# Performance work log

Hardware: AMD Instinct MI355X
Metric: run time of the kernel (lower is better)

## Reference

```python
import jax, jax.numpy as jnp
import numpy as np

EPS = 1e-5

def _layernorm(x, gamma, beta):
    mu = jnp.mean(x, axis=-1, keepdims=True)
    var = jnp.mean(jnp.square(x - mu), axis=-1, keepdims=True)
    return (x - mu) * jax.lax.rsqrt(var + EPS) * gamma + beta

def setup_inputs() -> dict:
    key = jax.random.key(0)
    kx, kw = jax.random.split(key)
    N, D, BIT = 65536, 1024, 64
    X = jax.random.normal(kx, (N, D), dtype=jnp.float32)
    # xavier_uniform with gain=0.5 for weight [BIT, D]
    limit = 0.5 * np.sqrt(6.0 / (D + BIT))
    W = jax.random.uniform(kw, (BIT, D), minval=-limit, maxval=limit, dtype=jnp.float32)
    b = jnp.zeros((BIT,), dtype=jnp.float32)
    ln1_g = jnp.ones((D,), dtype=jnp.float32)
    ln1_b = jnp.zeros((D,), dtype=jnp.float32)
    ln2_g = jnp.ones((BIT,), dtype=jnp.float32)
    ln2_b = jnp.zeros((BIT,), dtype=jnp.float32)
    return {"X": X, "W": W, "b": b, "ln1_g": ln1_g, "ln1_b": ln1_b, "ln2_g": ln2_g, "ln2_b": ln2_b}

def reference(X, W, b, ln1_g, ln1_b, ln2_g, ln2_b):
    # LayerNorm -> Linear -> LayerNorm
    xn = _layernorm(X, ln1_g, ln1_b)                       # [N, D]
    logits = jnp.einsum('nd,bd->nb', xn, W) + b            # [N, BIT]
    logits = _layernorm(logits, ln2_g, ln2_b)
    # mean-center over batch, tanh, sign-binarize
    logits = logits - jnp.mean(logits, axis=0, keepdims=True)
    H = jnp.tanh(0.5 * logits)
    B = jnp.where(H >= 0.0, jnp.int8(1), jnp.int8(-1))
    return H, B
```

## Files before the change

kernel.cpp:

```cpp
#include <hip/hip_runtime.h>
#include <stdint.h>

#define N_ROWS 65536
#define D_IN   1024
#define NBIT   64
#define LN_EPS 1e-5f

typedef __attribute__((ext_vector_type(8))) _Float16 f16x8;
typedef __attribute__((ext_vector_type(4))) float f32x4;

__device__ __forceinline__ void gload_lds16(const void* g, void* l) {
    __builtin_amdgcn_global_load_lds(
        (const __attribute__((address_space(1))) uint32_t*)g,
        (__attribute__((address_space(3))) uint32_t*)l, 16, 0, 0);
}

__device__ __forceinline__ f32x4 mfma16(f16x8 a, f16x8 b, f32x4 c) {
    return __builtin_amdgcn_mfma_f32_16x16x32_f16(a, b, c, 0, 0, 0);
}

__device__ __forceinline__ void do_tstep(float4 x0, float4 x1,
        const _Float16* bhp, f32x4* acc_h, f32x4* acc_m, f32x4* acc_ll,
        float& sum, float& sumsq) {
    float xs[8] = {x0.x, x0.y, x0.z, x0.w, x1.x, x1.y, x1.z, x1.w};
    f16x8 ahi, alo;
#pragma unroll
    for (int j = 0; j < 8; ++j) {
        float xv = xs[j];
        sum += xv;
        sumsq = fmaf(xv, xv, sumsq);
        _Float16 h = (_Float16)xv;
        ahi[j] = h;
        alo[j] = (_Float16)((xv - (float)h) * 2048.0f);
    }
#pragma unroll
    for (int nt = 0; nt < 4; ++nt) {
        f16x8 bh = *(const f16x8*)(bhp + nt * 512);
        f16x8 bl = *(const f16x8*)(bhp + 4096 + nt * 512);
        acc_h[nt]  = mfma16(ahi, bh, acc_h[nt]);
        acc_m[nt]  = mfma16(ahi, bl, acc_m[nt]);
        acc_m[nt]  = mfma16(alo, bh, acc_m[nt]);
        acc_ll[nt] = mfma16(alo, bl, acc_ll[nt]);
    }
}

__global__ void prep_kernel(const float* __restrict__ W, const float* __restrict__ bias,
                            const float* __restrict__ g1, const float* __restrict__ b1,
                            _Float16* __restrict__ whi, _Float16* __restrict__ wlo,
                            float* __restrict__ u, float* __restrict__ v) {
    int bit = blockIdx.x;
    int t   = threadIdx.x;
    int nt  = bit >> 4, bl = bit & 15;
    float su = 0.f, sv = 0.f;
    for (int d = t; d < D_IN; d += 256) {
        float w  = W[bit * D_IN + d];
        float gw = w * g1[d];
        su += gw;
        sv += w * b1[d];
        int kt = d >> 5, gg = (d >> 3) & 3, j = d & 7;
        size_t idx = (((size_t)(kt * 4 + nt)) * 64 + gg * 16 + bl) * 8 + j;
        _Float16 h = (_Float16)gw;
        whi[idx] = h;
        wlo[idx] = (_Float16)((gw - (float)h) * 2048.0f);
    }
    __shared__ float s1[256], s2[256];
    s1[t] = su; s2[t] = sv;
    __syncthreads();
    for (int off = 128; off > 0; off >>= 1) {
        if (t < off) { s1[t] += s1[t + off]; s2[t] += s2[t + off]; }
        __syncthreads();
    }
    if (t == 0) { u[bit] = s1[0]; v[bit] = s2[0] + bias[bit]; }
}

__global__ void __launch_bounds__(256) main_kernel(
        const float* __restrict__ X,
        const _Float16* __restrict__ whi, const _Float16* __restrict__ wlo,
        const float* __restrict__ u, const float* __restrict__ v,
        const float* __restrict__ g2, const float* __restrict__ b2,
        float* __restrict__ L, float* __restrict__ P) {
    __shared__ _Float16 lw[2][8192];
    int tid  = threadIdx.x;
    int wid  = tid >> 6, lane = tid & 63;
    int g    = lane >> 4, r16 = lane & 15;
    int row_base = blockIdx.x * 64 + wid * 16;

    const float* xrow = X + (size_t)(row_base + r16) * D_IN + g * 8;

    const _Float16* gbase = ((wid & 2) ? wlo : whi) + (wid & 1) * 2048 + lane * 8;
    const int lofs = ((wid & 2) ? 4096 : 0) + (wid & 1) * 2048;

#define STAGEW(cc, buf) do {                                         \
        const _Float16* gs_ = gbase + (cc) * 4096;                   \
        _Float16* ld_ = &lw[buf][lofs];                              \
        gload_lds16(gs_,         ld_);                               \
        gload_lds16(gs_ + 512,   ld_ + 512);                         \
        gload_lds16(gs_ + 1024,  ld_ + 1024);                        \
        gload_lds16(gs_ + 1536,  ld_ + 1536);                        \
    } while (0)

#define PREFX(cc, r0, r1, r2, r3) do {                               \
        const float* xp_ = xrow + (cc) * 64;                         \
        r0 = *(const float4*)(xp_);                                  \
        r1 = *(const float4*)(xp_ + 4);                              \
        r2 = *(const float4*)(xp_ + 32);                             \
        r3 = *(const float4*)(xp_ + 36);                             \
    } while (0)

    f32x4 acc_h0[4], acc_h1[4], acc_m[4], acc_ll[4];
#pragma unroll
    for (int nt = 0; nt < 4; ++nt) {
        acc_h0[nt] = (f32x4){0.f, 0.f, 0.f, 0.f};
        acc_h1[nt] = (f32x4){0.f, 0.f, 0.f, 0.f};
        acc_m[nt]  = (f32x4){0.f, 0.f, 0.f, 0.f};
        acc_ll[nt] = (f32x4){0.f, 0.f, 0.f, 0.f};
    }
    float sum = 0.f, sumsq = 0.f;
    float4 xa0, xa1, xa2, xa3, xb0, xb1, xb2, xb3;

    PREFX(0, xa0, xa1, xa2, xa3);
    STAGEW(0, 0);
    __syncthreads();

    for (int c2 = 0; c2 < 8; ++c2) {
        int c = 2 * c2;
        PREFX(c + 1, xb0, xb1, xb2, xb3);
        STAGEW(c + 1, 1);
        {
            const _Float16* bhp = &lw[0][0] + lane * 8;
            do_tstep(xa0, xa1, bhp,        acc_h0, acc_m, acc_ll, sum, sumsq);
            do_tstep(xa2, xa3, bhp + 2048, acc_h1, acc_m, acc_ll, sum, sumsq);
        }
        __syncthreads();
        if (c2 < 7) {
            PREFX(c + 2, xa0, xa1, xa2, xa3);
            STAGEW(c + 2, 0);
        }
        {
            const _Float16* bhp = &lw[1][0] + lane * 8;
            do_tstep(xb0, xb1, bhp,        acc_h0, acc_m, acc_ll, sum, sumsq);
            do_tstep(xb2, xb3, bhp + 2048, acc_h1, acc_m, acc_ll, sum, sumsq);
        }
        __syncthreads();
    }

    sum   += __shfl_xor(sum, 16);   sum   += __shfl_xor(sum, 32);
    sumsq += __shfl_xor(sumsq, 16); sumsq += __shfl_xor(sumsq, 32);
    float mu   = sum * (1.f / 1024.f);
    float var  = sumsq * (1.f / 1024.f) - mu * mu;
    float rstd = rsqrtf(var + LN_EPS);

    float uv[4], vv[4], g2v[4], b2v[4];
#pragma unroll
    for (int nt = 0; nt < 4; ++nt) {
        int bitc = nt * 16 + r16;
        uv[nt] = u[bitc]; vv[nt] = v[bitc]; g2v[nt] = g2[bitc]; b2v[nt] = b2[bitc];
    }
    float mu_m[4], rs_m[4];
#pragma unroll
    for (int reg = 0; reg < 4; ++reg) {
        int m = g * 4 + reg;
        mu_m[reg] = __shfl(mu, m);
        rs_m[reg] = __shfl(rstd, m);
    }

    float lg[4][4];
#pragma unroll
    for (int nt = 0; nt < 4; ++nt)
#pragma unroll
        for (int reg = 0; reg < 4; ++reg) {
            float dot = (acc_h0[nt][reg] + acc_h1[nt][reg])
                      + acc_m[nt][reg] * (1.0f / 2048.0f)
                      + acc_ll[nt][reg] * (1.0f / 4194304.0f);
            lg[nt][reg] = rs_m[reg] * dot - rs_m[reg] * mu_m[reg] * uv[nt] + vv[nt];
        }

#pragma unroll
    for (int reg = 0; reg < 4; ++reg) {
        float s1 = lg[0][reg] + lg[1][reg] + lg[2][reg] + lg[3][reg];
        float s2 = lg[0][reg]*lg[0][reg] + lg[1][reg]*lg[1][reg]
                 + lg[2][reg]*lg[2][reg] + lg[3][reg]*lg[3][reg];
#pragma unroll
        for (int m = 1; m <= 8; m <<= 1) {
            s1 += __shfl_xor(s1, m);
            s2 += __shfl_xor(s2, m);
        }
        float mean = s1 * (1.f / 64.f);
        float va   = s2 * (1.f / 64.f) - mean * mean;
        float rs2  = rsqrtf(va + LN_EPS);
#pragma unroll
        for (int nt = 0; nt < 4; ++nt)
            lg[nt][reg] = (lg[nt][reg] - mean) * rs2 * g2v[nt] + b2v[nt];
    }

#pragma unroll
    for (int reg = 0; reg < 4; ++reg) {
        size_t row = (size_t)(row_base + g * 4 + reg);
#pragma unroll
        for (int nt = 0; nt < 4; ++nt)
            L[row * 64 + nt * 16 + r16] = lg[nt][reg];
    }

#pragma unroll
    for (int nt = 0; nt < 4; ++nt) {
        float cs = lg[nt][0] + lg[nt][1] + lg[nt][2] + lg[nt][3];
        cs += __shfl_xor(cs, 16);
        cs += __shfl_xor(cs, 32);
        if (g == 0)
            P[(size_t)(nt * 16 + r16) * 4096 + blockIdx.x * 4 + wid] = cs;
    }
#undef STAGEW
#undef PREFX
}

__global__ void reduce_kernel(const float* __restrict__ P, float* __restrict__ cm) {
    int bit = blockIdx.x, t = threadIdx.x;
    float s = 0.f;
    for (int p = t; p < 4096; p += 256) s += P[(size_t)bit * 4096 + p];
    __shared__ float sh[256];
    sh[t] = s;
    __syncthreads();
    for (int off = 128; off > 0; off >>= 1) {
        if (t < off) sh[t] += sh[t + off];
        __syncthreads();
    }
    if (t == 0) cm[bit] = sh[0] * (1.f / (float)N_ROWS);
}

__global__ void final_kernel(const float* __restrict__ L, const float* __restrict__ cm,
                             float* __restrict__ out) {
    __shared__ float cms[64];
    if (threadIdx.x < 64) cms[threadIdx.x] = cm[threadIdx.x];
    __syncthreads();
    const float4* L4 = (const float4*)L;
    float4* H4 = (float4*)out;
    float4* B4 = (float4*)(out + (size_t)N_ROWS * NBIT);
    int total = N_ROWS * NBIT / 4;
    for (int i = blockIdx.x * blockDim.x + threadIdx.x; i < total;
         i += gridDim.x * blockDim.x) {
        float4 x = L4[i];
        int bb = (i & 15) * 4;
        float4 h, bo;
        h.x = tanhf(0.5f * (x.x - cms[bb + 0]));
        h.y = tanhf(0.5f * (x.y - cms[bb + 1]));
        h.z = tanhf(0.5f * (x.z - cms[bb + 2]));
        h.w = tanhf(0.5f * (x.w - cms[bb + 3]));
        bo.x = h.x >= 0.f ? 1.f : -1.f;
        bo.y = h.y >= 0.f ? 1.f : -1.f;
        bo.z = h.z >= 0.f ? 1.f : -1.f;
        bo.w = h.w >= 0.f ? 1.f : -1.f;
        H4[i] = h;
        B4[i] = bo;
    }
}

extern "C" void kernel_launch(void* const* d_in, const int* in_sizes, int n_in,
                              void* d_out, int out_size, void* d_ws, size_t ws_size,
                              hipStream_t stream) {
    (void)in_sizes; (void)n_in; (void)out_size; (void)ws_size;
    const float* X  = (const float*)d_in[0];
    const float* W  = (const float*)d_in[1];
    const float* bb = (const float*)d_in[2];
    const float* g1 = (const float*)d_in[3];
    const float* b1 = (const float*)d_in[4];
    const float* g2 = (const float*)d_in[5];
    const float* b2 = (const float*)d_in[6];

    char* ws = (char*)d_ws;
    _Float16* whi = (_Float16*)ws;
    _Float16* wlo = (_Float16*)(ws + 131072);
    float* u  = (float*)(ws + 262144);
    float* v  = (float*)(ws + 266240);
    float* P  = (float*)(ws + 270336);
    float* cm = (float*)(ws + 270336 + 64 * 4096 * 4);

    float* out = (float*)d_out;
    float* L   = out + (size_t)N_ROWS * NBIT;

    prep_kernel<<<64, 256, 0, stream>>>(W, bb, g1, b1, whi, wlo, u, v);
    main_kernel<<<1024, 256, 0, stream>>>(X, whi, wlo, u, v, g2, b2, L, P);
    reduce_kernel<<<64, 256, 0, stream>>>(P, cm);
    final_kernel<<<2048, 256, 0, stream>>>(L, cm, out);
}
```

Before: 98.09 us.

## Restructure main loop pipeline with explicit vmcnt waits and sched barriers

Rewrites the double-buffered K loop so X register prefetch runs two chunks ahead and W LDS staging one chunk ahead. Full __syncthreads (which drain all outstanding loads) are replaced with s_waitcnt vmcnt(4) plus s_barrier, so the next chunk's X loads can stay in flight across the barrier. Sched barriers pin the instruction order so the compiler cannot undo the overlap. This relies on precise vmcnt accounting of the outstanding loads; a wrong count would race on LDS.

```diff
diff --git a/kernel.cpp b/kernel.cpp
--- a/kernel.cpp
+++ b/kernel.cpp
@@ -107,6 +107,8 @@
         r3 = *(const float4*)(xp_ + 36);                             \
     } while (0)
 
+#define SB0 __builtin_amdgcn_sched_barrier(0)
+
     f32x4 acc_h0[4], acc_h1[4], acc_m[4], acc_ll[4];
 #pragma unroll
     for (int nt = 0; nt < 4; ++nt) {
@@ -119,29 +121,47 @@
     float4 xa0, xa1, xa2, xa3, xb0, xb1, xb2, xb3;
 
     PREFX(0, xa0, xa1, xa2, xa3);
+    PREFX(1, xb0, xb1, xb2, xb3);
     STAGEW(0, 0);
-    __syncthreads();
-
-    for (int c2 = 0; c2 < 8; ++c2) {
+    SB0;
+    asm volatile("s_waitcnt vmcnt(0)" ::: "memory");
+    __builtin_amdgcn_s_barrier();
+
+#define ITER(c, xr0, xr1, xr2, xr3) do {                                      \
+        STAGEW((c) + 1, ((c) + 1) & 1);                                       \
+        SB0;                                                                  \
+        {                                                                     \
+            const _Float16* bhp = &lw[(c) & 1][0] + lane * 8;                 \
+            do_tstep(xr0, xr1, bhp,        acc_h0, acc_m, acc_ll, sum, sumsq);\
+            do_tstep(xr2, xr3, bhp + 2048, acc_h1, acc_m, acc_ll, sum, sumsq);\
+        }                                                                     \
+        SB0;                                                                  \
+        PREFX((c) + 2, xr0, xr1, xr2, xr3);                                   \
+        SB0;                                                                  \
+        asm volatile("s_waitcnt vmcnt(4)" ::: "memory");                      \
+        __builtin_amdgcn_s_barrier();                                         \
+    } while (0)
+
+    for (int c2 = 0; c2 < 7; ++c2) {
         int c = 2 * c2;
-        PREFX(c + 1, xb0, xb1, xb2, xb3);
-        STAGEW(c + 1, 1);
-        {
-            const _Float16* bhp = &lw[0][0] + lane * 8;
-            do_tstep(xa0, xa1, bhp,        acc_h0, acc_m, acc_ll, sum, sumsq);
-            do_tstep(xa2, xa3, bhp + 2048, acc_h1, acc_m, acc_ll, sum, sumsq);
-        }
-        __syncthreads();
-        if (c2 < 7) {
-            PREFX(c + 2, xa0, xa1, xa2, xa3);
-            STAGEW(c + 2, 0);
-        }
-        {
-            const _Float16* bhp = &lw[1][0] + lane * 8;
-            do_tstep(xb0, xb1, bhp,        acc_h0, acc_m, acc_ll, sum, sumsq);
-            do_tstep(xb2, xb3, bhp + 2048, acc_h1, acc_m, acc_ll, sum, sumsq);
-        }
-        __syncthreads();
+        ITER(c,     xa0, xa1, xa2, xa3);
+        ITER(c + 1, xb0, xb1, xb2, xb3);
+    }
+
+    STAGEW(15, 1);
+    SB0;
+    {
+        const _Float16* bhp = &lw[0][0] + lane * 8;
+        do_tstep(xa0, xa1, bhp,        acc_h0, acc_m, acc_ll, sum, sumsq);
+        do_tstep(xa2, xa3, bhp + 2048, acc_h1, acc_m, acc_ll, sum, sumsq);
+    }
+    SB0;
+    asm volatile("s_waitcnt vmcnt(0)" ::: "memory");
+    __builtin_amdgcn_s_barrier();
+    {
+        const _Float16* bhp = &lw[1][0] + lane * 8;
+        do_tstep(xb0, xb1, bhp,        acc_h0, acc_m, acc_ll, sum, sumsq);
+        do_tstep(xb2, xb3, bhp + 2048, acc_h1, acc_m, acc_ll, sum, sumsq);
     }
 
     sum   += __shfl_xor(sum, 16);   sum   += __shfl_xor(sum, 32);
@@ -211,6 +231,8 @@
     }
 #undef STAGEW
 #undef PREFX
+#undef ITER
+#undef SB0
 }
 
 __global__ void reduce_kernel(const float* __restrict__ P, float* __restrict__ cm) {
```

Measured after the change: 98.21 us. About the same (+0.1%).

## Use 1024-thread blocks sharing staged weights, drop X register prefetch, add nontemporal loads/stores

Applied to the files above, without the earlier changes.

The main kernel now runs 256 blocks of 1024 threads (16 waves, 256 rows each), so each staged weight chunk in LDS is reused by four times as many rows and each thread issues only one LDS-bound load per chunk. The explicit X register double-buffering is replaced by direct nontemporal loads inside the loop, and L/H/B writes and L reads use nontemporal hints. This cuts weight staging traffic and register pressure, but X load latency is no longer hidden by software prefetch and relies on 16 waves per block instead. The larger blocks may also reduce occupancy flexibility and make each per-chunk barrier more costly.

```diff
diff --git a/kernel.cpp b/kernel.cpp
--- a/kernel.cpp
+++ b/kernel.cpp
@@ -15,14 +15,18 @@
         (__attribute__((address_space(3))) uint32_t*)l, 16, 0, 0);
 }
 
+__device__ __forceinline__ f32x4 ntload4(const float* p) {
+    return __builtin_nontemporal_load((const f32x4*)p);
+}
+
 __device__ __forceinline__ f32x4 mfma16(f16x8 a, f16x8 b, f32x4 c) {
     return __builtin_amdgcn_mfma_f32_16x16x32_f16(a, b, c, 0, 0, 0);
 }
 
-__device__ __forceinline__ void do_tstep(float4 x0, float4 x1,
+__device__ __forceinline__ void do_tstep(f32x4 x0, f32x4 x1,
         const _Float16* bhp, f32x4* acc_h, f32x4* acc_m, f32x4* acc_ll,
         float& sum, float& sumsq) {
-    float xs[8] = {x0.x, x0.y, x0.z, x0.w, x1.x, x1.y, x1.z, x1.w};
+    float xs[8] = {x0[0], x0[1], x0[2], x0[3], x1[0], x1[1], x1[2], x1[3]};
     f16x8 ahi, alo;
 #pragma unroll
     for (int j = 0; j < 8; ++j) {
@@ -73,7 +77,7 @@
     if (t == 0) { u[bit] = s1[0]; v[bit] = s2[0] + bias[bit]; }
 }
 
-__global__ void __launch_bounds__(256) main_kernel(
+__global__ void __launch_bounds__(1024) main_kernel(
         const float* __restrict__ X,
         const _Float16* __restrict__ whi, const _Float16* __restrict__ wlo,
         const float* __restrict__ u, const float* __restrict__ v,
@@ -83,29 +87,14 @@
     int tid  = threadIdx.x;
     int wid  = tid >> 6, lane = tid & 63;
     int g    = lane >> 4, r16 = lane & 15;
-    int row_base = blockIdx.x * 64 + wid * 16;
+    int row_base = blockIdx.x * 256 + wid * 16;
 
     const float* xrow = X + (size_t)(row_base + r16) * D_IN + g * 8;
 
-    const _Float16* gbase = ((wid & 2) ? wlo : whi) + (wid & 1) * 2048 + lane * 8;
-    const int lofs = ((wid & 2) ? 4096 : 0) + (wid & 1) * 2048;
-
-#define STAGEW(cc, buf) do {                                         \
-        const _Float16* gs_ = gbase + (cc) * 4096;                   \
-        _Float16* ld_ = &lw[buf][lofs];                              \
-        gload_lds16(gs_,         ld_);                               \
-        gload_lds16(gs_ + 512,   ld_ + 512);                         \
-        gload_lds16(gs_ + 1024,  ld_ + 1024);                        \
-        gload_lds16(gs_ + 1536,  ld_ + 1536);                        \
-    } while (0)
-
-#define PREFX(cc, r0, r1, r2, r3) do {                               \
-        const float* xp_ = xrow + (cc) * 64;                         \
-        r0 = *(const float4*)(xp_);                                  \
-        r1 = *(const float4*)(xp_ + 4);                              \
-        r2 = *(const float4*)(xp_ + 32);                             \
-        r3 = *(const float4*)(xp_ + 36);                             \
-    } while (0)
+    const _Float16* gsrc = ((wid & 8) ? wlo : whi) + (wid & 7) * 512 + (size_t)lane * 8;
+    const int ldst = ((wid & 8) ? 4096 : 0) + (wid & 7) * 512;
+
+#define STAGEW(cc, buf) gload_lds16(gsrc + (size_t)(cc) * 4096, &lw[buf][ldst])
 
     f32x4 acc_h0[4], acc_h1[4], acc_m[4], acc_ll[4];
 #pragma unroll
@@ -116,31 +105,20 @@
         acc_ll[nt] = (f32x4){0.f, 0.f, 0.f, 0.f};
     }
     float sum = 0.f, sumsq = 0.f;
-    float4 xa0, xa1, xa2, xa3, xb0, xb1, xb2, xb3;
-
-    PREFX(0, xa0, xa1, xa2, xa3);
+
     STAGEW(0, 0);
     __syncthreads();
 
-    for (int c2 = 0; c2 < 8; ++c2) {
-        int c = 2 * c2;
-        PREFX(c + 1, xb0, xb1, xb2, xb3);
-        STAGEW(c + 1, 1);
-        {
-            const _Float16* bhp = &lw[0][0] + lane * 8;
-            do_tstep(xa0, xa1, bhp,        acc_h0, acc_m, acc_ll, sum, sumsq);
-            do_tstep(xa2, xa3, bhp + 2048, acc_h1, acc_m, acc_ll, sum, sumsq);
-        }
-        __syncthreads();
-        if (c2 < 7) {
-            PREFX(c + 2, xa0, xa1, xa2, xa3);
-            STAGEW(c + 2, 0);
-        }
-        {
-            const _Float16* bhp = &lw[1][0] + lane * 8;
-            do_tstep(xb0, xb1, bhp,        acc_h0, acc_m, acc_ll, sum, sumsq);
-            do_tstep(xb2, xb3, bhp + 2048, acc_h1, acc_m, acc_ll, sum, sumsq);
-        }
+    for (int c = 0; c < 16; ++c) {
+        if (c < 15) STAGEW(c + 1, (c + 1) & 1);
+        int t = c * 2;
+        f32x4 x00 = ntload4(xrow + t * 32);
+        f32x4 x01 = ntload4(xrow + t * 32 + 4);
+        f32x4 x10 = ntload4(xrow + t * 32 + 32);
+        f32x4 x11 = ntload4(xrow + t * 32 + 36);
+        const _Float16* bhp = &lw[c & 1][0] + lane * 8;
+        do_tstep(x00, x01, bhp,        acc_h0, acc_m, acc_ll, sum, sumsq);
+        do_tstep(x10, x11, bhp + 2048, acc_h1, acc_m, acc_ll, sum, sumsq);
         __syncthreads();
     }
 
@@ -198,7 +176,7 @@
         size_t row = (size_t)(row_base + g * 4 + reg);
 #pragma unroll
         for (int nt = 0; nt < 4; ++nt)
-            L[row * 64 + nt * 16 + r16] = lg[nt][reg];
+            __builtin_nontemporal_store(lg[nt][reg], &L[row * 64 + nt * 16 + r16]);
     }
 
 #pragma unroll
@@ -207,10 +185,9 @@
         cs += __shfl_xor(cs, 16);
         cs += __shfl_xor(cs, 32);
         if (g == 0)
-            P[(size_t)(nt * 16 + r16) * 4096 + blockIdx.x * 4 + wid] = cs;
+            P[(size_t)(nt * 16 + r16) * 4096 + blockIdx.x * 16 + wid] = cs;
     }
 #undef STAGEW
-#undef PREFX
 }
 
 __global__ void reduce_kernel(const float* __restrict__ P, float* __restrict__ cm) {
@@ -232,25 +209,22 @@
     __shared__ float cms[64];
     if (threadIdx.x < 64) cms[threadIdx.x] = cm[threadIdx.x];
     __syncthreads();
-    const float4* L4 = (const float4*)L;
-    float4* H4 = (float4*)out;
-    float4* B4 = (float4*)(out + (size_t)N_ROWS * NBIT);
+    const f32x4* L4 = (const f32x4*)L;
+    f32x4* H4 = (f32x4*)out;
+    f32x4* B4 = (f32x4*)(out + (size_t)N_ROWS * NBIT);
     int total = N_ROWS * NBIT / 4;
     for (int i = blockIdx.x * blockDim.x + threadIdx.x; i < total;
          i += gridDim.x * blockDim.x) {
-        float4 x = L4[i];
+        f32x4 x = __builtin_nontemporal_load(&L4[i]);
         int bb = (i & 15) * 4;
-        float4 h, bo;
-        h.x = tanhf(0.5f * (x.x - cms[bb + 0]));
-        h.y = tanhf(0.5f * (x.y - cms[bb + 1]));
-        h.z = tanhf(0.5f * (x.z - cms[bb + 2]));
-        h.w = tanhf(0.5f * (x.w - cms[bb + 3]));
-        bo.x = h.x >= 0.f ? 1.f : -1.f;
-        bo.y = h.y >= 0.f ? 1.f : -1.f;
-        bo.z = h.z >= 0.f ? 1.f : -1.f;
-        bo.w = h.w >= 0.f ? 1.f : -1.f;
-        H4[i] = h;
-        B4[i] = bo;
+        f32x4 h, bo;
+#pragma unroll
+        for (int j = 0; j < 4; ++j) {
+            h[j]  = tanhf(0.5f * (x[j] - cms[bb + j]));
+            bo[j] = h[j] >= 0.f ? 1.f : -1.f;
+        }
+        __builtin_nontemporal_store(h, &H4[i]);
+        __builtin_nontemporal_store(bo, &B4[i]);
     }
 }
 
@@ -278,7 +252,7 @@
     float* L   = out + (size_t)N_ROWS * NBIT;
 
     prep_kernel<<<64, 256, 0, stream>>>(W, bb, g1, b1, whi, wlo, u, v);
-    main_kernel<<<1024, 256, 0, stream>>>(X, whi, wlo, u, v, g2, b2, L, P);
+    main_kernel<<<256, 1024, 0, stream>>>(X, whi, wlo, u, v, g2, b2, L, P);
     reduce_kernel<<<64, 256, 0, stream>>>(P, cm);
     final_kernel<<<2048, 256, 0, stream>>>(L, cm, out);
 }
```

New measurement: 100.6 us. +2.5%, slower.
